# Kernel optimization log

Hardware: AMD Instinct MI355X
Metric: run time of the kernel (lower is better)

## Reference

```python
import jax, jax.numpy as jnp
from jax import lax
import numpy as np

G, NPG = 256, 512            # graphs, nodes per graph
N, E = G * NPG, 1048576      # total nodes, total edges
F, DE = 26, 52               # node feat dim, edge attr dim
NL = 2                       # num_layers
L = DE * (NL - 1) + 1        # latent_dim = 53 == F*NL + 1
K = 128                      # sort-pool k
HID, DH = 32, 512            # hidden (conv1d_2 out channels), dense_hidden
Z = 2 * F + DE               # CGConv gate input dim


def setup_inputs():
    ks = jax.random.split(jax.random.key(0), 24)
    x = jax.random.normal(ks[0], (N, F), jnp.float32)
    eg = jax.random.randint(ks[1], (E,), 0, G)
    src = eg * NPG + jax.random.randint(ks[2], (E,), 0, NPG)
    dst = eg * NPG + jax.random.randint(ks[3], (E,), 0, NPG)
    edge_index = jnp.stack([src, dst]).astype(jnp.int32)
    edge_attr = jax.random.normal(ks[4], (E, DE), jnp.float32)
    batch = jnp.repeat(jnp.arange(G, dtype=jnp.int32), NPG)
    interface_pos = jnp.arange(N, dtype=jnp.int32)
    interface_count = jax.random.uniform(ks[5], (N, 1), jnp.float32)
    def lin(k, o, i):
        return jax.random.normal(k, (o, i), jnp.float32) * 0.05
    return dict(
        x=x, edge_attr=edge_attr, interface_count=interface_count,
        Wf1=lin(ks[6], F, Z), bf1=jnp.zeros((F,), jnp.float32),
        Ws1=lin(ks[7], F, Z), bs1=jnp.zeros((F,), jnp.float32),
        Wf2=lin(ks[8], F, Z), bf2=jnp.zeros((F,), jnp.float32),
        Ws2=lin(ks[9], F, Z), bs2=jnp.zeros((F,), jnp.float32),
        Wc1=jax.random.normal(ks[10], (16, 1, L), jnp.float32) * 0.05,
        bc1=jnp.zeros((16,), jnp.float32),
        Wc2=jax.random.normal(ks[11], (32, 16, 5), jnp.float32) * 0.05,
        bc2=jnp.zeros((32,), jnp.float32),
        W0=lin(ks[12], DH, (K // 2 - 4) * HID), b0=jnp.zeros((DH,), jnp.float32),
        W1=lin(ks[13], DH // 2, DH), b1=jnp.zeros((DH // 2,), jnp.float32),
        W2=lin(ks[14], 1, DH // 2), b2=jnp.zeros((1,), jnp.float32),
        edge_index=edge_index, batch=batch, interface_pos=interface_pos,
        graph_num=G)


def _cgconv(x, edge_index, edge_attr, Wf, bf, Ws, bs):
    # PyG CGConv: x_i' = x_i + sum_j sigmoid(W_f z_ij + b_f) * softplus(W_s z_ij + b_s)
    src, dst = edge_index[0], edge_index[1]  # x_j = src, x_i = dst
    z = jnp.concatenate([x[dst], x[src], edge_attr], axis=-1)  # [E, 2F+DE]
    msg = jax.nn.sigmoid(z @ Wf.T + bf) * jax.nn.softplus(z @ Ws.T + bs)
    return x + jax.ops.segment_sum(msg, dst, num_segments=x.shape[0])


def _forward(x, edge_attr, interface_count, Wf1, bf1, Ws1, bs1, Wf2, bf2, Ws2, bs2,
             Wc1, bc1, Wc2, bc2, W0, b0, W1, b1, W2, b2,
             edge_index, interface_pos, graph_num):
    h1 = jnp.tanh(_cgconv(x, edge_index, edge_attr, Wf1, bf1, Ws1, bs1))
    h2 = jnp.tanh(_cgconv(h1, edge_index, edge_attr, Wf2, bf2, Ws2, bs2))
    # per-graph softmax of interface_count (graphs are contiguous, equal-sized)
    s = jax.nn.softmax(interface_count.reshape(graph_num, NPG), axis=1).reshape(N, 1)
    xcat = jnp.concatenate([h1, h2, s], axis=-1)[interface_pos]  # JumpingKnowledge cat, [N, L]
    # global_sort_pool: per graph, sort nodes by last channel descending, keep top K
    xg = xcat.reshape(graph_num, NPG, L)
    order = jnp.argsort(-xg[..., -1], axis=1)[:, :K]           # [G, K]
    pooled = jnp.take_along_axis(xg, order[..., None], axis=1)  # [G, K, L]
    # conv1d(1->16, kernel=stride=L) over [G,1,K*L] == per-pooled-node linear
    h = jax.nn.relu(jnp.einsum('gkl,ol->gok', pooled, Wc1[:, 0, :]) + bc1[None, :, None])
    h = h.reshape(graph_num, 16, K // 2, 2).max(axis=-1)        # MaxPool1d(2,2)
    h = lax.conv_general_dilated(h, Wc2, window_strides=(1,), padding='VALID',
                                 dimension_numbers=('NCH', 'OIH', 'NCH'))
    h = jax.nn.relu(h + bc2[None, :, None])                     # [G, 32, K//2-4]
    h = h.reshape(graph_num, -1)
    h = jax.nn.relu(h @ W0.T + b0)
    h = jax.nn.relu(h @ W1.T + b1)  # dropout p=0.5 is identity in eval mode
    return h @ W2.T + b2            # [G, 1]


def reference(x, edge_attr, interface_count, Wf1, bf1, Ws1, bs1, Wf2, bf2, Ws2, bs2,
              Wc1, bc1, Wc2, bc2, W0, b0, W1, b1, W2, b2,
              edge_index, batch, interface_pos, graph_num):
    return _forward(x, edge_attr, interface_count, Wf1, bf1, Ws1, bs1, Wf2, bf2, Ws2, bs2,
                    Wc1, bc1, Wc2, bc2, W0, b0, W1, b1, W2, b2,
                    edge_index, interface_pos, graph_num)
```

## Files before the change

kernel.cpp:

```cpp
#include <hip/hip_runtime.h>
#include <hip/hip_bf16.h>

#define GG 256
#define NPG 512
#define NN (GG*NPG)
#define EE 1048576
#define FF 26
#define DEA 52
#define KK 128

__global__ __launch_bounds__(256) void node_proj_k(
    const float* __restrict__ x, const float* __restrict__ Wf,
    const float* __restrict__ Ws, float* __restrict__ pdst,
    float* __restrict__ psrc) {
  int idx = blockIdx.x * 256 + threadIdx.x;
  if (idx >= NN * 52) return;
  int n = idx / 52, j = idx % 52;
  const float* W = (j < 26) ? Wf : Ws;
  int o = (j < 26) ? j : j - 26;
  const float* xr = x + n * FF;
  const float* wd = W + o * 104;
  const float* wsp = W + o * 104 + 26;
  float ad = 0.f, as = 0.f;
#pragma unroll
  for (int c = 0; c < FF; ++c) {
    float xv = xr[c];
    ad = fmaf(wd[c], xv, ad);
    as = fmaf(wsp[c], xv, as);
  }
  pdst[idx] = ad;
  psrc[n * 52 + j] = as;
}

__global__ __launch_bounds__(256) void edge_k(
    const int* __restrict__ ei, const float* __restrict__ ea,
    const float* __restrict__ pdst, const float* __restrict__ psrc,
    const float* __restrict__ Wf, const float* __restrict__ bf,
    const float* __restrict__ Ws, const float* __restrict__ bs,
    float* __restrict__ acc) {
  __shared__ alignas(16) float ealds[32 * 56];
  __shared__ int dsts[32], srcs[32];
  int tid = threadIdx.x;
  int e0 = blockIdx.x * 32;
  if (tid < 32) {
    srcs[tid] = ei[e0 + tid];
    dsts[tid] = ei[EE + e0 + tid];
  }
  for (int f = tid; f < 32 * 52; f += 256) {
    int e = f / 52, i = f % 52;
    ealds[e * 56 + i] = ea[(size_t)e0 * 52 + f];
  }
  int o = tid & 31;
  int oc = (o < 26) ? o : 0;
  float wfr[52], wsr[52];
  const float* wfp = Wf + oc * 104 + 52;
  const float* wsp = Ws + oc * 104 + 52;
#pragma unroll
  for (int i = 0; i < 52; ++i) { wfr[i] = wfp[i]; wsr[i] = wsp[i]; }
  float bfv = bf[oc], bsv = bs[oc];
  __syncthreads();
  int slot = tid >> 5;
  for (int t = 0; t < 4; ++t) {
    int el = t * 8 + slot;
    int dst = dsts[el], src = srcs[el];
    float yf = bfv, ys = bsv;
    const float4* ar = (const float4*)&ealds[el * 56];
#pragma unroll
    for (int u = 0; u < 13; ++u) {
      float4 a = ar[u];
      yf = fmaf(wfr[4*u+0], a.x, yf); ys = fmaf(wsr[4*u+0], a.x, ys);
      yf = fmaf(wfr[4*u+1], a.y, yf); ys = fmaf(wsr[4*u+1], a.y, ys);
      yf = fmaf(wfr[4*u+2], a.z, yf); ys = fmaf(wsr[4*u+2], a.z, ys);
      yf = fmaf(wfr[4*u+3], a.w, yf); ys = fmaf(wsr[4*u+3], a.w, ys);
    }
    yf += pdst[(size_t)dst * 52 + oc] + psrc[(size_t)src * 52 + oc];
    ys += pdst[(size_t)dst * 52 + 26 + oc] + psrc[(size_t)src * 52 + 26 + oc];
    float sg = 1.0f / (1.0f + __expf(-yf));
    float sp = fmaxf(ys, 0.0f) + log1pf(__expf(-fabsf(ys)));
    float msg = sg * sp;
    if (o < 26) atomicAdd(&acc[(size_t)dst * FF + o], msg);
  }
}

__global__ __launch_bounds__(256) void upd_k(const float* __restrict__ xin,
                                             const float* __restrict__ acc,
                                             float* __restrict__ h) {
  int i = blockIdx.x * 256 + threadIdx.x;
  h[i] = tanhf(xin[i] + acc[i]);
}

__global__ __launch_bounds__(512) void softmax_k(const float* __restrict__ ic,
                                                 float* __restrict__ s) {
  int g = blockIdx.x, j = threadIdx.x;
  __shared__ float red[512];
  float v = ic[g * NPG + j];
  red[j] = v; __syncthreads();
  for (int off = 256; off > 0; off >>= 1) {
    if (j < off) red[j] = fmaxf(red[j], red[j + off]);
    __syncthreads();
  }
  float mx = red[0]; __syncthreads();
  float e = expf(v - mx);
  red[j] = e; __syncthreads();
  for (int off = 256; off > 0; off >>= 1) {
    if (j < off) red[j] += red[j + off];
    __syncthreads();
  }
  s[g * NPG + j] = e / red[0];
}

__global__ __launch_bounds__(256) void transpose_k(const float* __restrict__ A,
                                                   float* __restrict__ AT,
                                                   int R, int C) {
  int idx = blockIdx.x * 256 + threadIdx.x;
  if (idx >= R * C) return;
  int r = idx / C, c = idx % C;
  AT[c * R + r] = A[idx];
}

__global__ __launch_bounds__(512) void head_k(
    const float* __restrict__ h1, const float* __restrict__ h2,
    const float* __restrict__ s_arr, const int* __restrict__ ipos,
    const float* __restrict__ Wc1, const float* __restrict__ bc1,
    const float* __restrict__ Wc2, const float* __restrict__ bc2,
    const float* __restrict__ W0T, const float* __restrict__ b0,
    const float* __restrict__ W1T, const float* __restrict__ b1,
    const float* __restrict__ W2, const float* __restrict__ b2,
    float* __restrict__ out) {
  int g = blockIdx.x, tid = threadIdx.x;
  __shared__ float kbuf[512];
  __shared__ int order[128];
  __shared__ float pooled[128][57];
  __shared__ float out1[16][128];
  __shared__ float mpool[16][64];
  __shared__ float h2c[1920];
  __shared__ float d0[512];
  __shared__ float d1[256];

  int nj = ipos[g * NPG + tid];
  kbuf[tid] = s_arr[nj];
  __syncthreads();
  float kj = kbuf[tid];
  int rank = 0;
  for (int t = 0; t < 512; ++t) {
    float kt = kbuf[t];
    rank += (kt > kj) || (kt == kj && t < tid);
  }
  if (rank < KK) order[rank] = tid;
  __syncthreads();

  for (int f = tid; f < KK * 53; f += 512) {
    int k = f / 53, l = f % 53;
    int node = ipos[g * NPG + order[k]];
    float v = (l < 26) ? h1[(size_t)node * 26 + l]
                       : (l < 52 ? h2[(size_t)node * 26 + (l - 26)] : s_arr[node]);
    pooled[k][l] = v;
  }
  __syncthreads();

  for (int p = tid; p < 16 * 128; p += 512) {
    int o = p >> 7, k = p & 127;
    float a = bc1[o];
    for (int l = 0; l < 53; ++l) a = fmaf(pooled[k][l], Wc1[o * 53 + l], a);
    out1[o][k] = fmaxf(a, 0.f);
  }
  __syncthreads();

  for (int p = tid; p < 16 * 64; p += 512) {
    int o = p >> 6, q = p & 63;
    mpool[o][q] = fmaxf(out1[o][2 * q], out1[o][2 * q + 1]);
  }
  __syncthreads();

  for (int p = tid; p < 32 * 60; p += 512) {
    int o = p / 60, q = p % 60;
    float a = bc2[o];
    for (int c = 0; c < 16; ++c)
#pragma unroll
      for (int t5 = 0; t5 < 5; ++t5)
        a = fmaf(mpool[c][q + t5], Wc2[(o * 16 + c) * 5 + t5], a);
    h2c[o * 60 + q] = fmaxf(a, 0.f);
  }
  __syncthreads();

  {
    float a = b0[tid];
    for (int q = 0; q < 1920; ++q) a = fmaf(h2c[q], W0T[q * 512 + tid], a);
    d0[tid] = fmaxf(a, 0.f);
  }
  __syncthreads();

  if (tid < 256) {
    float a = b1[tid];
    for (int q = 0; q < 512; ++q) a = fmaf(d0[q], W1T[q * 256 + tid], a);
    d1[tid] = fmaxf(a, 0.f);
  }
  __syncthreads();

  if (tid < 256) kbuf[tid] = d1[tid] * W2[tid];
  __syncthreads();
  if (tid < 64) {
    float v = kbuf[tid] + kbuf[tid + 64] + kbuf[tid + 128] + kbuf[tid + 192];
    for (int off = 32; off > 0; off >>= 1) v += __shfl_down(v, off);
    if (tid == 0) out[g] = v + b2[0];
  }
}

extern "C" void kernel_launch(void* const* d_in, const int* in_sizes, int n_in,
                              void* d_out, int out_size, void* d_ws, size_t ws_size,
                              hipStream_t stream) {
  const float* x    = (const float*)d_in[0];
  const float* ea   = (const float*)d_in[1];
  const float* ic   = (const float*)d_in[2];
  const float* Wf1  = (const float*)d_in[3];
  const float* bf1  = (const float*)d_in[4];
  const float* Ws1  = (const float*)d_in[5];
  const float* bs1  = (const float*)d_in[6];
  const float* Wf2  = (const float*)d_in[7];
  const float* bf2  = (const float*)d_in[8];
  const float* Ws2  = (const float*)d_in[9];
  const float* bs2  = (const float*)d_in[10];
  const float* Wc1  = (const float*)d_in[11];
  const float* bc1  = (const float*)d_in[12];
  const float* Wc2  = (const float*)d_in[13];
  const float* bc2  = (const float*)d_in[14];
  const float* W0   = (const float*)d_in[15];
  const float* b0   = (const float*)d_in[16];
  const float* W1   = (const float*)d_in[17];
  const float* b1   = (const float*)d_in[18];
  const float* W2   = (const float*)d_in[19];
  const float* b2   = (const float*)d_in[20];
  const int*   ei   = (const int*)d_in[21];
  const int*   ipos = (const int*)d_in[23];
  float* out = (float*)d_out;

  const size_t N26 = (size_t)NN * 26;
  const size_t N52 = (size_t)NN * 52;
  float* ws = (float*)d_ws;
  float* acc  = ws;
  float* h1   = acc + N26;
  float* h2   = h1 + N26;
  float* pdst = h2 + N26;
  float* psrc = pdst + N52;
  float* sarr = psrc + N52;
  float* W0T  = sarr + NN;
  float* W1T  = W0T + 1920 * 512;

  hipMemsetAsync(acc, 0, N26 * sizeof(float), stream);
  node_proj_k<<<(NN * 52) / 256, 256, 0, stream>>>(x, Wf1, Ws1, pdst, psrc);
  edge_k<<<EE / 32, 256, 0, stream>>>(ei, ea, pdst, psrc, Wf1, bf1, Ws1, bs1, acc);
  upd_k<<<(NN * 26) / 256, 256, 0, stream>>>(x, acc, h1);
  hipMemsetAsync(acc, 0, N26 * sizeof(float), stream);
  node_proj_k<<<(NN * 52) / 256, 256, 0, stream>>>(h1, Wf2, Ws2, pdst, psrc);
  edge_k<<<EE / 32, 256, 0, stream>>>(ei, ea, pdst, psrc, Wf2, bf2, Ws2, bs2, acc);
  upd_k<<<(NN * 26) / 256, 256, 0, stream>>>(h1, acc, h2);
  softmax_k<<<GG, 512, 0, stream>>>(ic, sarr);
  transpose_k<<<(512 * 1920) / 256, 256, 0, stream>>>(W0, W0T, 512, 1920);
  transpose_k<<<(256 * 512) / 256, 256, 0, stream>>>(W1, W1T, 256, 512);
  head_k<<<GG, 512, 0, stream>>>(h1, h2, sarr, ipos, Wc1, bc1, Wc2, bc2,
                                 W0T, b0, W1T, b1, W2, b2, out);
}
```

Baseline: 1.468 ms.

## Interleave node projections per node and stage weights in shared memory

The node projection now writes one 104-float row per node, holding dst and src projections for both gates, so each edge's dst and src gathers each touch a single contiguous row. Projection weights are transposed into LDS once per block, and the edge kernel loads its weight registers from an LDS transposed copy instead of strided global reads. This aims to cut scattered gather traffic and uncoalesced weight loads. The cost is extra LDS staging work in every block, a redundant weight transpose in each of the many edge blocks, and twice as many projection threads, each doing half the work.

Measured after the change: 1.824 ms. 24.2% more time.

```diff
diff --git a/kernel.cpp b/kernel.cpp
--- a/kernel.cpp
+++ b/kernel.cpp
@@ -6,39 +6,38 @@
 #define NN (GG*NPG)
 #define EE 1048576
 #define FF 26
-#define DEA 52
 #define KK 128
 
-__global__ __launch_bounds__(256) void node_proj_k(
+__global__ __launch_bounds__(256) void proj_k(
     const float* __restrict__ x, const float* __restrict__ Wf,
-    const float* __restrict__ Ws, float* __restrict__ pdst,
-    float* __restrict__ psrc) {
-  int idx = blockIdx.x * 256 + threadIdx.x;
-  if (idx >= NN * 52) return;
-  int n = idx / 52, j = idx % 52;
-  const float* W = (j < 26) ? Wf : Ws;
-  int o = (j < 26) ? j : j - 26;
+    const float* __restrict__ Ws, float* __restrict__ p) {
+  __shared__ float wT[26 * 113];
+  int tid = threadIdx.x;
+  for (int t = tid; t < 4 * 26 * 26; t += 256) {
+    int q = t / 676, r = t % 676, o = r / 26, c = r % 26;
+    const float* W = (q & 1) ? Ws : Wf;
+    int col = (q >> 1) ? (26 + c) : c;
+    wT[c * 113 + q * 26 + o] = W[o * 104 + col];
+  }
+  __syncthreads();
+  int idx = blockIdx.x * 256 + tid;
+  if (idx >= NN * 104) return;
+  int n = idx / 104, j = idx % 104;
   const float* xr = x + n * FF;
-  const float* wd = W + o * 104;
-  const float* wsp = W + o * 104 + 26;
-  float ad = 0.f, as = 0.f;
-#pragma unroll
-  for (int c = 0; c < FF; ++c) {
-    float xv = xr[c];
-    ad = fmaf(wd[c], xv, ad);
-    as = fmaf(wsp[c], xv, as);
-  }
-  pdst[idx] = ad;
-  psrc[n * 52 + j] = as;
+  float a = 0.f;
+#pragma unroll
+  for (int c = 0; c < FF; ++c) a = fmaf(xr[c], wT[c * 113 + j], a);
+  p[idx] = a;
 }
 
 __global__ __launch_bounds__(256) void edge_k(
     const int* __restrict__ ei, const float* __restrict__ ea,
-    const float* __restrict__ pdst, const float* __restrict__ psrc,
+    const float* __restrict__ p,
     const float* __restrict__ Wf, const float* __restrict__ bf,
     const float* __restrict__ Ws, const float* __restrict__ bs,
     float* __restrict__ acc) {
   __shared__ alignas(16) float ealds[32 * 56];
+  __shared__ float weT[52 * 66];
   __shared__ int dsts[32], srcs[32];
   int tid = threadIdx.x;
   int e0 = blockIdx.x * 32;
@@ -46,19 +45,25 @@
     srcs[tid] = ei[e0 + tid];
     dsts[tid] = ei[EE + e0 + tid];
   }
+  for (int t = tid; t < 2 * 26 * 52; t += 256) {
+    int m = t / 1352, r = t % 1352, o = r / 52, i = r % 52;
+    const float* W = m ? Ws : Wf;
+    weT[i * 66 + m * 33 + o] = W[o * 104 + 52 + i];
+  }
   for (int f = tid; f < 32 * 52; f += 256) {
     int e = f / 52, i = f % 52;
     ealds[e * 56 + i] = ea[(size_t)e0 * 52 + f];
   }
   int o = tid & 31;
   int oc = (o < 26) ? o : 0;
+  float bfv = bf[oc], bsv = bs[oc];
+  __syncthreads();
   float wfr[52], wsr[52];
-  const float* wfp = Wf + oc * 104 + 52;
-  const float* wsp = Ws + oc * 104 + 52;
-#pragma unroll
-  for (int i = 0; i < 52; ++i) { wfr[i] = wfp[i]; wsr[i] = wsp[i]; }
-  float bfv = bf[oc], bsv = bs[oc];
-  __syncthreads();
+#pragma unroll
+  for (int i = 0; i < 52; ++i) {
+    wfr[i] = weT[i * 66 + oc];
+    wsr[i] = weT[i * 66 + 33 + oc];
+  }
   int slot = tid >> 5;
   for (int t = 0; t < 4; ++t) {
     int el = t * 8 + slot;
@@ -73,8 +78,10 @@
       yf = fmaf(wfr[4*u+2], a.z, yf); ys = fmaf(wsr[4*u+2], a.z, ys);
       yf = fmaf(wfr[4*u+3], a.w, yf); ys = fmaf(wsr[4*u+3], a.w, ys);
     }
-    yf += pdst[(size_t)dst * 52 + oc] + psrc[(size_t)src * 52 + oc];
-    ys += pdst[(size_t)dst * 52 + 26 + oc] + psrc[(size_t)src * 52 + 26 + oc];
+    const float* pd = p + (size_t)dst * 104;
+    const float* ps = p + (size_t)src * 104;
+    yf += pd[oc] + ps[52 + oc];
+    ys += pd[26 + oc] + ps[78 + oc];
     float sg = 1.0f / (1.0f + __expf(-yf));
     float sp = fmaxf(ys, 0.0f) + log1pf(__expf(-fabsf(ys)));
     float msg = sg * sp;
@@ -234,25 +241,24 @@
   const int*   ipos = (const int*)d_in[23];
   float* out = (float*)d_out;
 
-  const size_t N26 = (size_t)NN * 26;
-  const size_t N52 = (size_t)NN * 52;
+  const size_t N26  = (size_t)NN * 26;
+  const size_t N104 = (size_t)NN * 104;
   float* ws = (float*)d_ws;
   float* acc  = ws;
   float* h1   = acc + N26;
   float* h2   = h1 + N26;
-  float* pdst = h2 + N26;
-  float* psrc = pdst + N52;
-  float* sarr = psrc + N52;
+  float* p    = h2 + N26;
+  float* sarr = p + N104;
   float* W0T  = sarr + NN;
   float* W1T  = W0T + 1920 * 512;
 
   hipMemsetAsync(acc, 0, N26 * sizeof(float), stream);
-  node_proj_k<<<(NN * 52) / 256, 256, 0, stream>>>(x, Wf1, Ws1, pdst, psrc);
-  edge_k<<<EE / 32, 256, 0, stream>>>(ei, ea, pdst, psrc, Wf1, bf1, Ws1, bs1, acc);
+  proj_k<<<(NN * 104) / 256, 256, 0, stream>>>(x, Wf1, Ws1, p);
+  edge_k<<<EE / 32, 256, 0, stream>>>(ei, ea, p, Wf1, bf1, Ws1, bs1, acc);
   upd_k<<<(NN * 26) / 256, 256, 0, stream>>>(x, acc, h1);
   hipMemsetAsync(acc, 0, N26 * sizeof(float), stream);
-  node_proj_k<<<(NN * 52) / 256, 256, 0, stream>>>(h1, Wf2, Ws2, pdst, psrc);
-  edge_k<<<EE / 32, 256, 0, stream>>>(ei, ea, pdst, psrc, Wf2, bf2, Ws2, bs2, acc);
+  proj_k<<<(NN * 104) / 256, 256, 0, stream>>>(h1, Wf2, Ws2, p);
+  edge_k<<<EE / 32, 256, 0, stream>>>(ei, ea, p, Wf2, bf2, Ws2, bs2, acc);
   upd_k<<<(NN * 26) / 256, 256, 0, stream>>>(h1, acc, h2);
   softmax_k<<<GG, 512, 0, stream>>>(ic, sarr);
   transpose_k<<<(512 * 1920) / 256, 256, 0, stream>>>(W0, W0T, 512, 1920);
```
